# Performance work log

Measured on AMD Instinct MI355X. Metric: run time of the kernel, lower is better.

The kernel has to match this reference:

```python
import jax, jax.numpy as jnp
import numpy as np

B, SEQ, DIM = 1, 2048, 4096
N_HEADS, N_KV, HEAD_DIM = 32, 8, 128
N_REP = N_HEADS // N_KV
MAX_CTX = 4096


def setup_inputs() -> dict:
    key = jax.random.key(0)
    ks = jax.random.split(key, 6)
    x = jax.random.normal(ks[0], (B, SEQ, DIM), jnp.float32)
    # RoPE table: (1, SEQ, 1, HEAD_DIM//2, 2) with [cos, sin] in last dim
    inv_freq = 1.0 / (10000.0 ** (jnp.arange(0, HEAD_DIM, 2, dtype=jnp.float32) / HEAD_DIM))
    t = jnp.arange(SEQ, dtype=jnp.float32)
    ang = t[:, None] * inv_freq[None, :]
    freqs_cis = jnp.stack([jnp.cos(ang), jnp.sin(ang)], axis=-1).reshape(1, SEQ, 1, HEAD_DIM // 2, 2)
    cache_kv = jnp.zeros((2, 1, MAX_CTX, N_KV, HEAD_DIM), jnp.float32)
    s = 0.02
    wq = jax.random.normal(ks[1], (DIM, N_HEADS * HEAD_DIM), jnp.float32) * s
    wk = jax.random.normal(ks[2], (DIM, N_KV * HEAD_DIM), jnp.float32) * s
    wv = jax.random.normal(ks[3], (DIM, N_KV * HEAD_DIM), jnp.float32) * s
    wo = jax.random.normal(ks[4], (N_HEADS * HEAD_DIM, DIM), jnp.float32) * s
    return {"x": x, "cache_kv": cache_kv, "freqs_cis": freqs_cis,
            "wq": wq, "wk": wk, "wv": wv, "wo": wo, "start_pos": 0}


def _rope(t, freqs_cis):
    # t: (b, s, h, head_dim); freqs_cis: (1, s, 1, head_dim//2, 2)
    tr = t.reshape(*t.shape[:-1], -1, 2)
    a, b = tr[..., 0], tr[..., 1]
    c, d = freqs_cis[..., 0], freqs_cis[..., 1]
    return jnp.stack([a * c - b * d, a * d + b * c], axis=-1).reshape(t.shape)


def reference(x, cache_kv, freqs_cis, wq, wk, wv, wo, start_pos):
    b, s, _ = x.shape
    xq = (x @ wq).reshape(b, s, N_HEADS, HEAD_DIM)
    xk = (x @ wk).reshape(b, s, N_KV, HEAD_DIM)
    xv = (x @ wv).reshape(b, s, N_KV, HEAD_DIM)
    xq = _rope(xq, freqs_cis)
    xk = _rope(xk, freqs_cis)
    # KV-cache scatter write (start_pos is a static Python int)
    cache = cache_kv.at[:, :, start_pos:start_pos + s].set(jnp.stack([xk, xv]))
    L = start_pos + s
    keys = cache[0, :, :L]    # (b, L, kv, hd)
    values = cache[1, :, :L]
    # GQA without materializing repeats: group q heads by kv head
    q = xq.transpose(0, 2, 1, 3).reshape(b, N_KV, N_REP, s, HEAD_DIM)
    k = keys.transpose(0, 2, 1, 3)     # (b, kv, L, hd)
    v = values.transpose(0, 2, 1, 3)
    scores = jnp.einsum('bkrqd,bkld->bkrql', q, k) * (HEAD_DIM ** -0.5)
    if s > 1:
        mask = jnp.triu(jnp.full((s, L), -jnp.inf, jnp.float32), k=start_pos + 1)
        scores = scores + mask
    p = jax.nn.softmax(scores, axis=-1)
    out = jnp.einsum('bkrql,bkld->bkrqd', p, v)          # (b, kv, rep, s, hd)
    out = out.reshape(b, N_HEADS, s, HEAD_DIM).transpose(0, 2, 1, 3).reshape(b, s, N_HEADS * HEAD_DIM)
    return out @ wo
```

## Files before the change

### kernel.cpp

```cpp
#include <hip/hip_runtime.h>
#include <hip/hip_bf16.h>
#include <stdint.h>

#define SEQ   2048
#define DIM   4096
#define NH    32
#define NKV   8
#define HD    128
#define NREP  4
#define QKVN  6144
#define KOFF  4096
#define VOFF  5120

typedef __bf16 bf16;
typedef __attribute__((ext_vector_type(8))) __bf16 bf16x8;
typedef __attribute__((ext_vector_type(4))) __bf16 bf16x4;
typedef __attribute__((ext_vector_type(4))) float  f32x4;
typedef __attribute__((address_space(1))) void as1_void;
typedef __attribute__((address_space(3))) void as3_void;

__device__ __forceinline__ void async_copy16(void* lds, const void* g) {
  __builtin_amdgcn_global_load_lds((as1_void*)(void*)g, (as3_void*)lds, 16, 0, 0);
}

__device__ __forceinline__ uint32_t pack2bf(float a, float b) {
  union { bf16 h; uint16_t u; } ca, cb;
  ca.h = (bf16)a; cb.h = (bf16)b;
  return (uint32_t)ca.u | ((uint32_t)cb.u << 16);
}

__global__ __launch_bounds__(256) void cast_x_kernel(const float* __restrict__ src,
                                                     bf16* __restrict__ dst) {
  size_t i = ((size_t)blockIdx.x * 256 + threadIdx.x) * 4;
  const float4 v = *(const float4*)(src + i);
  bf16x4 o;
  o[0] = (bf16)v.x; o[1] = (bf16)v.y; o[2] = (bf16)v.z; o[3] = (bf16)v.w;
  *(bf16x4*)(dst + i) = o;
}

__global__ __launch_bounds__(256) void transpose_cast_kernel(const float* __restrict__ src,
                                                             bf16* __restrict__ dst,
                                                             int R, int C) {
  __shared__ float tile[32][33];
  int c0 = blockIdx.x * 32, r0 = blockIdx.y * 32;
  int tx = threadIdx.x & 31, ty = threadIdx.x >> 5;
#pragma unroll
  for (int j = 0; j < 4; ++j)
    tile[ty + j*8][tx] = src[(size_t)(r0 + ty + j*8) * C + c0 + tx];
  __syncthreads();
  int g = threadIdx.x >> 4;
  int k = threadIdx.x & 15;
#pragma unroll
  for (int jj = 0; jj < 2; ++jj) {
    int X  = g + jj*16;
    int Y0 = k*2;
    uint32_t pv = pack2bf(tile[Y0][X], tile[Y0+1][X]);
    *(uint32_t*)&dst[(size_t)(c0 + X) * R + r0 + Y0] = pv;
  }
}

template<int OUT_F32>
__global__ __launch_bounds__(256) void gemm_bt_kernel(const bf16* __restrict__ A,
                                                      const bf16* __restrict__ Bt,
                                                      void* __restrict__ Cout,
                                                      int M, int N, int K) {
  __shared__ __align__(16) bf16 As[128*32];
  __shared__ __align__(16) bf16 Bs[128*32];
  const int tid = threadIdx.x;
  const int w = tid >> 6, lane = tid & 63;
  const int lane16 = lane & 15, quad = lane >> 4;
  const int wr = w >> 1, wc = w & 1;
  const int bm = blockIdx.y * 128, bn = blockIdx.x * 128;
  const bf16* a0 = A  + (size_t)bm * K;
  const bf16* b0 = Bt + (size_t)bn * K;
  f32x4 acc[4][4] = {};
  for (int k0 = 0; k0 < K; k0 += 32) {
    __syncthreads();
#pragma unroll
    for (int i = 0; i < 2; ++i) {
      int c = tid + i * 256;
      async_copy16(&As[c*8], a0 + (size_t)(c >> 2) * K + k0 + (c & 3) * 8);
      async_copy16(&Bs[c*8], b0 + (size_t)(c >> 2) * K + k0 + (c & 3) * 8);
    }
    __syncthreads();
    bf16x8 af[4];
#pragma unroll
    for (int i = 0; i < 4; ++i)
      af[i] = *(const bf16x8*)&As[(wr*64 + i*16 + lane16)*32 + quad*8];
#pragma unroll
    for (int j = 0; j < 4; ++j) {
      bf16x8 bfrag = *(const bf16x8*)&Bs[(wc*64 + j*16 + lane16)*32 + quad*8];
#pragma unroll
      for (int i = 0; i < 4; ++i)
        acc[i][j] = __builtin_amdgcn_mfma_f32_16x16x32_bf16(af[i], bfrag, acc[i][j], 0, 0, 0);
    }
  }
#pragma unroll
  for (int i = 0; i < 4; ++i)
#pragma unroll
    for (int j = 0; j < 4; ++j)
#pragma unroll
      for (int r = 0; r < 4; ++r) {
        size_t row = (size_t)bm + wr*64 + i*16 + quad*4 + r;
        size_t col = (size_t)bn + wc*64 + j*16 + lane16;
        float v = acc[i][j][r];
        if (OUT_F32) ((float*)Cout)[row * N + col] = v;
        else         ((bf16*)Cout)[row * N + col] = (bf16)v;
      }
}

__global__ __launch_bounds__(256) void rope_kernel(bf16* __restrict__ qkv,
                                                   const float* __restrict__ fr) {
  int idx = blockIdx.x * 256 + threadIdx.x;
  int p  = idx & 63;
  int hh = (idx >> 6) % 40;
  int t  = (idx >> 6) / 40;
  int col = (hh < NH) ? (hh * HD + 2*p) : (KOFF + (hh - NH) * HD + 2*p);
  float c = fr[((size_t)t*64 + p)*2 + 0];
  float d = fr[((size_t)t*64 + p)*2 + 1];
  bf16* ptr = qkv + (size_t)t * QKVN + col;
  float a = (float)ptr[0], b = (float)ptr[1];
  ptr[0] = (bf16)(a*c - b*d);
  ptr[1] = (bf16)(a*d + b*c);
}

__global__ __launch_bounds__(256) void transpose_v_kernel(const bf16* __restrict__ qkv,
                                                          bf16* __restrict__ vt) {
  __shared__ bf16 tile[32][33];
  int tt = blockIdx.x * 32;
  int dd = blockIdx.y * 32;
  int kv = blockIdx.z;
  int tx = threadIdx.x & 31, ty = threadIdx.x >> 5;
  const bf16* src = qkv + VOFF + kv * HD;
#pragma unroll
  for (int j = 0; j < 4; ++j)
    tile[ty + j*8][tx] = src[(size_t)(tt + ty + j*8) * QKVN + dd + tx];
  __syncthreads();
  bf16* dst = vt + ((size_t)kv * HD + dd) * SEQ + tt;
#pragma unroll
  for (int j = 0; j < 4; ++j)
    dst[(size_t)(ty + j*8) * SEQ + tx] = tile[tx][ty + j*8];
}

__global__ __launch_bounds__(256, 3) void flash_attn_kernel(const bf16* __restrict__ qkv,
                                                            const bf16* __restrict__ vt,
                                                            bf16* __restrict__ out) {
  __shared__ __align__(16) bf16 Ks[4*96*32];
  __shared__ __align__(16) bf16 Vts[3*128*32];
  const int b  = blockIdx.x;
  const int qt = 31 - (b >> 5);
  const int h  = b & 31;
  const int kvh = h >> 2;
  const int tid = threadIdx.x;
  const int w = tid >> 6, lane = tid & 63;
  const int lane16 = lane & 15, quad = lane >> 4;
  const float scale = 0.08838834764831845f;
  const int qglob = qt*64 + w*16 + lane16;

  const bf16* qrow = qkv + (size_t)qglob * QKVN + h * HD + quad*8;
  bf16x8 qreg[4];
#pragma unroll
  for (int kk = 0; kk < 4; ++kk)
    qreg[kk] = *(const bf16x8*)(qrow + kk*32);

  f32x4 acc_o[8] = {};
  float m_s = -3e38f, l_s = 0.f;

  const bf16* kbase0 = qkv + KOFF + kvh * HD;
  const bf16* vbase0 = vt + (size_t)kvh * HD * SEQ;

  const int L = (qt*64 + 159) / 96;
  for (int jj = 0; jj < L; ++jj) {
    const int kv0 = jj * 96;
    __syncthreads();
#pragma unroll
    for (int i = 0; i < 6; ++i) {
      int c = tid + i * 256;
      {
        int kk = c / 384, rem = c - kk*384;
        async_copy16(&Ks[c*8], kbase0 + (size_t)(kv0 + (rem >> 2)) * QKVN + kk*32 + (rem & 3) * 8);
      }
      {
        int kk2 = c >> 9, cp = c & 511;
        async_copy16(&Vts[c*8], vbase0 + (size_t)(cp >> 2) * SEQ + kv0 + kk2*32 + (cp & 3) * 8);
      }
    }
    __syncthreads();

    f32x4 accT[6] = {};
#pragma unroll
    for (int kk = 0; kk < 4; ++kk)
#pragma unroll
      for (int jn = 0; jn < 6; ++jn) {
        bf16x8 kf = *(const bf16x8*)&Ks[(kk*96 + jn*16 + lane16)*32 + quad*8];
        accT[jn] = __builtin_amdgcn_mfma_f32_16x16x32_bf16(kf, qreg[kk], accT[jn], 0, 0, 0);
      }

    float s[6][4];
#pragma unroll
    for (int jn = 0; jn < 6; ++jn)
#pragma unroll
      for (int r = 0; r < 4; ++r) {
        float v = accT[jn][r] * scale;
        if ((kv0 + jn*16 + quad*4 + r) > qglob) v = -3e38f;
        s[jn][r] = v;
      }

    float mt = s[0][0];
#pragma unroll
    for (int jn = 0; jn < 6; ++jn)
#pragma unroll
      for (int r = 0; r < 4; ++r) mt = fmaxf(mt, s[jn][r]);
    mt = fmaxf(mt, __shfl_xor(mt, 16));
    mt = fmaxf(mt, __shfl_xor(mt, 32));
    float mnew = fmaxf(m_s, mt);
    float alpha = __expf(m_s - mnew);
    m_s = mnew;
    float rs = 0.f;
#pragma unroll
    for (int jn = 0; jn < 6; ++jn)
#pragma unroll
      for (int r = 0; r < 4; ++r) {
        float p = __expf(s[jn][r] - mnew);
        s[jn][r] = p;
        rs += p;
      }
    rs += __shfl_xor(rs, 16);
    rs += __shfl_xor(rs, 32);
    l_s = l_s * alpha + rs;

    float alpha_row[4];
#pragma unroll
    for (int r = 0; r < 4; ++r)
      alpha_row[r] = __shfl(alpha, quad*4 + r);
#pragma unroll
    for (int jd = 0; jd < 8; ++jd)
#pragma unroll
      for (int r = 0; r < 4; ++r) acc_o[jd][r] *= alpha_row[r];

    uint32_t pk[6][2];
#pragma unroll
    for (int jn = 0; jn < 6; ++jn) {
      pk[jn][0] = pack2bf(s[jn][0], s[jn][1]);
      pk[jn][1] = pack2bf(s[jn][2], s[jn][3]);
    }

    const int src0 = (quad & 1) * 32 + lane16;
    const int src1 = src0 + 16;
    const bool hi = quad >= 2;
#pragma unroll
    for (int kk2 = 0; kk2 < 3; ++kk2) {
      uint32_t v0l = __shfl(pk[2*kk2][0],   src0), v0h = __shfl(pk[2*kk2][1],   src0);
      uint32_t v1l = __shfl(pk[2*kk2][0],   src1), v1h = __shfl(pk[2*kk2][1],   src1);
      uint32_t w0l = __shfl(pk[2*kk2+1][0], src0), w0h = __shfl(pk[2*kk2+1][1], src0);
      uint32_t w1l = __shfl(pk[2*kk2+1][0], src1), w1h = __shfl(pk[2*kk2+1][1], src1);
      union { uint32_t u[4]; bf16x8 v; } af;
      af.u[0] = hi ? w0l : v0l;
      af.u[1] = hi ? w0h : v0h;
      af.u[2] = hi ? w1l : v1l;
      af.u[3] = hi ? w1h : v1h;
#pragma unroll
      for (int jd = 0; jd < 8; ++jd) {
        bf16x8 vf = *(const bf16x8*)&Vts[(kk2*128 + jd*16 + lane16)*32 + quad*8];
        acc_o[jd] = __builtin_amdgcn_mfma_f32_16x16x32_bf16(af.v, vf, acc_o[jd], 0, 0, 0);
      }
    }
  }

  const float inv_l = 1.f / l_s;
  float linv[4];
#pragma unroll
  for (int r = 0; r < 4; ++r)
    linv[r] = __shfl(inv_l, quad*4 + r);

  bf16* obase = out + (size_t)(qt*64 + w*16) * DIM + h * HD;
#pragma unroll
  for (int jd = 0; jd < 8; ++jd)
#pragma unroll
    for (int r = 0; r < 4; ++r)
      obase[(size_t)(quad*4 + r) * DIM + jd*16 + lane16] = (bf16)(acc_o[jd][r] * linv[r]);
}

extern "C" void kernel_launch(void* const* d_in, const int* in_sizes, int n_in,
                              void* d_out, int out_size, void* d_ws, size_t ws_size,
                              hipStream_t stream) {
  const float* x  = (const float*)d_in[0];
  const float* fr = (const float*)d_in[2];
  const float* wq = (const float*)d_in[3];
  const float* wk = (const float*)d_in[4];
  const float* wv = (const float*)d_in[5];
  const float* wo = (const float*)d_in[6];
  float* out = (float*)d_out;

  char* ws = (char*)d_ws;
  bf16* xb     = (bf16*)(ws);
  bf16* wqkv_t = (bf16*)(ws + 16777216);
  bf16* wo_t   = (bf16*)(ws + 67108864);
  bf16* qkv    = (bf16*)(ws + 100663296);
  bf16* vt     = (bf16*)(ws + 125829120);
  bf16* attn   = (bf16*)(ws + 130023424);
  (void)ws_size; (void)in_sizes; (void)n_in; (void)out_size;

  cast_x_kernel<<<8192, 256, 0, stream>>>(x, xb);
  transpose_cast_kernel<<<dim3(128,128), 256, 0, stream>>>(wq, wqkv_t, DIM, DIM);
  transpose_cast_kernel<<<dim3(32,128),  256, 0, stream>>>(wk, wqkv_t + (size_t)4096*4096, DIM, 1024);
  transpose_cast_kernel<<<dim3(32,128),  256, 0, stream>>>(wv, wqkv_t + (size_t)5120*4096, DIM, 1024);
  transpose_cast_kernel<<<dim3(128,128), 256, 0, stream>>>(wo, wo_t, DIM, DIM);

  gemm_bt_kernel<0><<<dim3(48,16), 256, 0, stream>>>(xb, wqkv_t, qkv, SEQ, QKVN, DIM);
  rope_kernel<<<20480, 256, 0, stream>>>(qkv, fr);
  transpose_v_kernel<<<dim3(64,4,8), 256, 0, stream>>>(qkv, vt);
  flash_attn_kernel<<<1024, 256, 0, stream>>>(qkv, vt, attn);
  gemm_bt_kernel<1><<<dim3(32,16), 256, 0, stream>>>(attn, wo_t, out, SEQ, DIM, DIM);
}
```

Measured before the change: 569.8 us.

## Fuse RoPE into QKV GEMM epilogue, deepen K-step, vectorize weight transpose

Applies rotary embedding inside the QKV GEMM epilogue, using lane shuffles to pair elements, and removes the standalone rope kernel and its extra read/write pass over qkv. The GEMM now stages 64-wide K chunks per barrier pair to halve synchronization. The weight transpose-cast uses 64x64 tiles with float4 loads and 4-wide bf16 stores to improve memory efficiency. The larger LDS footprint may reduce occupancy.

```diff
diff --git a/kernel.cpp b/kernel.cpp
--- a/kernel.cpp
+++ b/kernel.cpp
@@ -41,31 +41,40 @@
 __global__ __launch_bounds__(256) void transpose_cast_kernel(const float* __restrict__ src,
                                                              bf16* __restrict__ dst,
                                                              int R, int C) {
-  __shared__ float tile[32][33];
-  int c0 = blockIdx.x * 32, r0 = blockIdx.y * 32;
-  int tx = threadIdx.x & 31, ty = threadIdx.x >> 5;
-#pragma unroll
-  for (int j = 0; j < 4; ++j)
-    tile[ty + j*8][tx] = src[(size_t)(r0 + ty + j*8) * C + c0 + tx];
+  __shared__ float tile[64][65];
+  const int c0 = blockIdx.x * 64, r0 = blockIdx.y * 64;
+  const int tx = threadIdx.x & 15, ty = threadIdx.x >> 4;
+#pragma unroll
+  for (int p = 0; p < 4; ++p) {
+    float4 v = *(const float4*)&src[(size_t)(r0 + ty + p*16) * C + c0 + tx*4];
+    tile[ty + p*16][tx*4+0] = v.x;
+    tile[ty + p*16][tx*4+1] = v.y;
+    tile[ty + p*16][tx*4+2] = v.z;
+    tile[ty + p*16][tx*4+3] = v.w;
+  }
   __syncthreads();
-  int g = threadIdx.x >> 4;
-  int k = threadIdx.x & 15;
-#pragma unroll
-  for (int jj = 0; jj < 2; ++jj) {
-    int X  = g + jj*16;
-    int Y0 = k*2;
-    uint32_t pv = pack2bf(tile[Y0][X], tile[Y0+1][X]);
-    *(uint32_t*)&dst[(size_t)(c0 + X) * R + r0 + Y0] = pv;
+  const int k = threadIdx.x & 15;
+  const int g = threadIdx.x >> 4;
+#pragma unroll
+  for (int p = 0; p < 4; ++p) {
+    int X = g + 16*p;
+    bf16x4 o;
+    o[0] = (bf16)tile[4*k+0][X];
+    o[1] = (bf16)tile[4*k+1][X];
+    o[2] = (bf16)tile[4*k+2][X];
+    o[3] = (bf16)tile[4*k+3][X];
+    *(bf16x4*)&dst[(size_t)(c0 + X) * R + r0 + 4*k] = o;
   }
 }
 
-template<int OUT_F32>
+template<int OUT_F32, int ROPE>
 __global__ __launch_bounds__(256) void gemm_bt_kernel(const bf16* __restrict__ A,
                                                       const bf16* __restrict__ Bt,
                                                       void* __restrict__ Cout,
-                                                      int M, int N, int K) {
-  __shared__ __align__(16) bf16 As[128*32];
-  __shared__ __align__(16) bf16 Bs[128*32];
+                                                      int M, int N, int K,
+                                                      const float* __restrict__ fr) {
+  __shared__ __align__(16) bf16 As[2*128*32];
+  __shared__ __align__(16) bf16 Bs[2*128*32];
   const int tid = threadIdx.x;
   const int w = tid >> 6, lane = tid & 63;
   const int lane16 = lane & 15, quad = lane >> 4;
@@ -74,54 +83,53 @@
   const bf16* a0 = A  + (size_t)bm * K;
   const bf16* b0 = Bt + (size_t)bn * K;
   f32x4 acc[4][4] = {};
-  for (int k0 = 0; k0 < K; k0 += 32) {
+  for (int k0 = 0; k0 < K; k0 += 64) {
     __syncthreads();
 #pragma unroll
-    for (int i = 0; i < 2; ++i) {
+    for (int i = 0; i < 4; ++i) {
       int c = tid + i * 256;
-      async_copy16(&As[c*8], a0 + (size_t)(c >> 2) * K + k0 + (c & 3) * 8);
-      async_copy16(&Bs[c*8], b0 + (size_t)(c >> 2) * K + k0 + (c & 3) * 8);
+      int kk = c >> 9, rem = c & 511;
+      async_copy16(&As[c*8], a0 + (size_t)(rem >> 2) * K + k0 + kk*32 + (rem & 3) * 8);
+      async_copy16(&Bs[c*8], b0 + (size_t)(rem >> 2) * K + k0 + kk*32 + (rem & 3) * 8);
     }
     __syncthreads();
-    bf16x8 af[4];
-#pragma unroll
-    for (int i = 0; i < 4; ++i)
-      af[i] = *(const bf16x8*)&As[(wr*64 + i*16 + lane16)*32 + quad*8];
+#pragma unroll
+    for (int kk = 0; kk < 2; ++kk) {
+      bf16x8 af[4];
+#pragma unroll
+      for (int i = 0; i < 4; ++i)
+        af[i] = *(const bf16x8*)&As[kk*4096 + (wr*64 + i*16 + lane16)*32 + quad*8];
+#pragma unroll
+      for (int j = 0; j < 4; ++j) {
+        bf16x8 bfrag = *(const bf16x8*)&Bs[kk*4096 + (wc*64 + j*16 + lane16)*32 + quad*8];
+#pragma unroll
+        for (int i = 0; i < 4; ++i)
+          acc[i][j] = __builtin_amdgcn_mfma_f32_16x16x32_bf16(af[i], bfrag, acc[i][j], 0, 0, 0);
+      }
+    }
+  }
+#pragma unroll
+  for (int i = 0; i < 4; ++i)
 #pragma unroll
     for (int j = 0; j < 4; ++j) {
-      bf16x8 bfrag = *(const bf16x8*)&Bs[(wc*64 + j*16 + lane16)*32 + quad*8];
-#pragma unroll
-      for (int i = 0; i < 4; ++i)
-        acc[i][j] = __builtin_amdgcn_mfma_f32_16x16x32_bf16(af[i], bfrag, acc[i][j], 0, 0, 0);
-    }
-  }
-#pragma unroll
-  for (int i = 0; i < 4; ++i)
-#pragma unroll
-    for (int j = 0; j < 4; ++j)
+      const bool do_rope = ROPE && (bn + wc*64 + j*16) < 5120;
+      const int p2 = (bn + wc*64 + j*16 + lane16) & 126;
 #pragma unroll
       for (int r = 0; r < 4; ++r) {
         size_t row = (size_t)bm + wr*64 + i*16 + quad*4 + r;
         size_t col = (size_t)bn + wc*64 + j*16 + lane16;
         float v = acc[i][j][r];
+        if (ROPE) {
+          float vp = __shfl_xor(v, 1);
+          if (do_rope) {
+            float2 cd = *(const float2*)&fr[row*128 + p2];
+            v = (lane16 & 1) ? (vp*cd.y + v*cd.x) : (v*cd.x - vp*cd.y);
+          }
+        }
         if (OUT_F32) ((float*)Cout)[row * N + col] = v;
         else         ((bf16*)Cout)[row * N + col] = (bf16)v;
       }
-}
-
-__global__ __launch_bounds__(256) void rope_kernel(bf16* __restrict__ qkv,
-                                                   const float* __restrict__ fr) {
-  int idx = blockIdx.x * 256 + threadIdx.x;
-  int p  = idx & 63;
-  int hh = (idx >> 6) % 40;
-  int t  = (idx >> 6) / 40;
-  int col = (hh < NH) ? (hh * HD + 2*p) : (KOFF + (hh - NH) * HD + 2*p);
-  float c = fr[((size_t)t*64 + p)*2 + 0];
-  float d = fr[((size_t)t*64 + p)*2 + 1];
-  bf16* ptr = qkv + (size_t)t * QKVN + col;
-  float a = (float)ptr[0], b = (float)ptr[1];
-  ptr[0] = (bf16)(a*c - b*d);
-  ptr[1] = (bf16)(a*d + b*c);
+    }
 }
 
 __global__ __launch_bounds__(256) void transpose_v_kernel(const bf16* __restrict__ qkv,
@@ -302,14 +310,13 @@
   (void)ws_size; (void)in_sizes; (void)n_in; (void)out_size;
 
   cast_x_kernel<<<8192, 256, 0, stream>>>(x, xb);
-  transpose_cast_kernel<<<dim3(128,128), 256, 0, stream>>>(wq, wqkv_t, DIM, DIM);
-  transpose_cast_kernel<<<dim3(32,128),  256, 0, stream>>>(wk, wqkv_t + (size_t)4096*4096, DIM, 1024);
-  transpose_cast_kernel<<<dim3(32,128),  256, 0, stream>>>(wv, wqkv_t + (size_t)5120*4096, DIM, 1024);
-  transpose_cast_kernel<<<dim3(128,128), 256, 0, stream>>>(wo, wo_t, DIM, DIM);
-
-  gemm_bt_kernel<0><<<dim3(48,16), 256, 0, stream>>>(xb, wqkv_t, qkv, SEQ, QKVN, DIM);
-  rope_kernel<<<20480, 256, 0, stream>>>(qkv, fr);
+  transpose_cast_kernel<<<dim3(64,64), 256, 0, stream>>>(wq, wqkv_t, DIM, DIM);
+  transpose_cast_kernel<<<dim3(16,64), 256, 0, stream>>>(wk, wqkv_t + (size_t)4096*4096, DIM, 1024);
+  transpose_cast_kernel<<<dim3(16,64), 256, 0, stream>>>(wv, wqkv_t + (size_t)5120*4096, DIM, 1024);
+  transpose_cast_kernel<<<dim3(64,64), 256, 0, stream>>>(wo, wo_t, DIM, DIM);
+
+  gemm_bt_kernel<0,1><<<dim3(48,16), 256, 0, stream>>>(xb, wqkv_t, qkv, SEQ, QKVN, DIM, fr);
   transpose_v_kernel<<<dim3(64,4,8), 256, 0, stream>>>(qkv, vt);
   flash_attn_kernel<<<1024, 256, 0, stream>>>(qkv, vt, attn);
-  gemm_bt_kernel<1><<<dim3(32,16), 256, 0, stream>>>(attn, wo_t, out, SEQ, DIM, DIM);
-}
+  gemm_bt_kernel<1,0><<<dim3(32,16), 256, 0, stream>>>(attn, wo_t, out, SEQ, DIM, DIM, nullptr);
+}
```

After: 551.6 us. -3.2%, faster.
